# Optimization experiments

Hardware: AMD Instinct MI355X
Metric: run time of the kernel (lower is better)

The kernel has to match this reference:

```python
import jax, jax.numpy as jnp
import numpy as np

NUM_SAMPLES = 32
PATCH = 3
GROUP = 8
NUM_RUNS = 1
BOUNDARY_SHARE = 0.7


def setup_inputs() -> dict:
    key = jax.random.key(0)
    k1, k2 = jax.random.split(key)
    fmap = jax.random.normal(k1, (2, 64, 64, 64, 64), dtype=jnp.float32)
    mask = jax.random.randint(k2, (2, 64, 64, 64), 0, 2).astype(jnp.int32)
    return {"fmap": fmap, "mask": mask}


def _sample_k(key, probs, fallback, k, num_runs):
    # probs, fallback: (N, S). Returns (N, num_runs, k) indices sampled with replacement.
    n = probs.shape[0]
    if k == 0:
        return jnp.zeros((n, num_runs, 0), dtype=jnp.int32)
    probs = jnp.clip(jnp.nan_to_num(probs), 0.0, None)
    fb = jnp.clip(jnp.nan_to_num(fallback), 0.0, None)
    fb = jnp.where(fb.sum(axis=1, keepdims=True) == 0, 1.0, fb)  # fallback uniform if fb empty
    probs = jnp.where(probs.sum(axis=1, keepdims=True) == 0, fb, probs)
    logits = jnp.log(probs)  # -inf on zero prob entries; categorical handles unnormalized logits
    idx = jax.random.categorical(key, logits, shape=(num_runs * k, n)).T  # (N, num_runs*k)
    return idx.reshape(n, num_runs, k)


def _unravel_center(idx, H, W, r, Hp, Wp):
    # idx: flat index into unpadded (D,H,W) volume -> flat index of center in padded volume
    z = idx // (H * W)
    rem = idx % (H * W)
    y = rem // W
    x = rem % W
    return (z + r) * (Hp * Wp) + (y + r) * Wp + (x + r)


def reference(fmap, mask):
    B, C, D, H, W = fmap.shape
    g = GROUP
    G = C // g
    p = PATCH
    r = p // 2
    p3 = p ** 3
    ns = NUM_SAMPLES
    R = NUM_RUNS
    boundary_k = int(ns * BOUNDARY_SHARE)
    rest_k = ns - boundary_k

    maskf = mask.astype(jnp.float32)
    # replicate-pad feature map
    fmap_pad = jnp.pad(fmap, ((0, 0), (0, 0), (r, r), (r, r), (r, r)), mode='edge')
    Dp, Hp, Wp = D + 2 * r, H + 2 * r, W + 2 * r
    S_p = Dp * Hp * Wp

    # valid centers (interior)
    valid = jnp.zeros((B, D, H, W), dtype=bool).at[:, r:D - r, r:H - r, r:W - r].set(True)

    # boundary detection via 3x3x3 ones conv over the mask
    kernel = jnp.ones((1, 1, p, p, p), jnp.float32)
    counts = jax.lax.conv_general_dilated(
        maskf[:, None], kernel, (1, 1, 1), [(r, r)] * 3,
        dimension_numbers=('NCDHW', 'OIDHW', 'NCDHW'))[:, 0]

    pos_b = ((mask == 1) & (counts < p3)).reshape(B, -1).astype(jnp.float32)
    neg_b = ((mask == 0) & (counts > 0)).reshape(B, -1).astype(jnp.float32)
    pos = (mask == 1).reshape(B, -1).astype(jnp.float32)
    neg = (mask == 0).reshape(B, -1).astype(jnp.float32)
    validf = valid.reshape(B, -1).astype(jnp.float32)

    rep = lambda m: jnp.repeat(m, G, axis=0)  # (B,S) -> (B*G,S)

    keys = jax.random.split(jax.random.key(42), 4)
    pos_idx = jnp.concatenate([
        _sample_k(keys[0], rep(pos_b), rep(pos), boundary_k, R),
        _sample_k(keys[1], rep(pos), rep(validf), rest_k, R)], axis=2)
    neg_idx = jnp.concatenate([
        _sample_k(keys[2], rep(neg_b), rep(neg), boundary_k, R),
        _sample_k(keys[3], rep(neg), rep(validf), rest_k, R)], axis=2)
    pos_idx = pos_idx.reshape(B, G, R, ns)
    neg_idx = neg_idx.reshape(B, G, R, ns)

    # 3x3x3 neighborhood flat offsets in the padded volume
    d = jnp.arange(-r, r + 1)
    offs = (d[:, None, None] * (Hp * Wp) + d[None, :, None] * Wp + d[None, None, :]).reshape(-1)

    def gather_patches(idx):
        center = _unravel_center(idx, H, W, r, Hp, Wp)  # (B,G,R,ns)
        idxs = center[..., None] + offs  # (B,G,R,ns,p3)
        idxs_flat = idxs.reshape(B, G, 1, R * ns * p3)
        src = fmap_pad.reshape(B, G, g, S_p)
        patches = jnp.take_along_axis(src, idxs_flat, axis=3)  # (B,G,g,R*ns*p3)
        patches = patches.reshape(B, G, g, R, ns, p3).transpose(0, 1, 3, 4, 2, 5)
        return patches.reshape(B, G, R, ns * g * p3)

    pos_out = gather_patches(pos_idx)
    neg_out = gather_patches(neg_idx)
    return jnp.concatenate([pos_out, neg_out], axis=3)  # (B,G,R, 2*ns*g*p3)
```

## Files before the change

### kernel.cpp

```cpp
#include <hip/hip_runtime.h>
#include <stdint.h>


#define S_VOL   262144
#define VALID_N 238328
#define OUT_N   221184
#define CTR(b, set) (((b) * 4 + (set)) * 16)

struct Keys { uint32_t k[4][2]; };

#define TF_ROUND(r) { x0 += x1; x1 = (x1 << (r)) | (x1 >> (32 - (r))); x1 ^= x0; }

__host__ __device__ static inline void tf2x32(uint32_t k0, uint32_t k1,
                                              uint32_t& x0, uint32_t& x1) {
  uint32_t ks2 = k0 ^ k1 ^ 0x1BD11BDAu;
  x0 += k0; x1 += k1;
  TF_ROUND(13) TF_ROUND(15) TF_ROUND(26) TF_ROUND(6)
  x0 += k1;  x1 += ks2 + 1u;
  TF_ROUND(17) TF_ROUND(29) TF_ROUND(16) TF_ROUND(24)
  x0 += ks2; x1 += k0 + 2u;
  TF_ROUND(13) TF_ROUND(15) TF_ROUND(26) TF_ROUND(6)
  x0 += k0;  x1 += k1 + 3u;
  TF_ROUND(17) TF_ROUND(29) TF_ROUND(16) TF_ROUND(24)
  x0 += k1;  x1 += ks2 + 4u;
  TF_ROUND(13) TF_ROUND(15) TF_ROUND(26) TF_ROUND(6)
  x0 += ks2; x1 += k0 + 5u;
}

#define ROTL(x, r) __builtin_amdgcn_alignbit((x), (x), 32u - (r))
#define R4(a,b,c,d) { x0+=x1; x1=ROTL(x1,a); x1^=x0; \
                      x0+=x1; x1=ROTL(x1,b); x1^=x0; \
                      x0+=x1; x1=ROTL(x1,c); x1^=x0; \
                      x0+=x1; x1=ROTL(x1,d); x1^=x0; }

struct TFC { uint32_t x0i, sk1, a1,b1,a2,b2,a3,b3,a4,b4,a5,b5; };

__device__ static inline uint32_t tf_hash(uint32_t s, const TFC& c) {
  uint32_t x0 = c.x0i, x1 = s + c.sk1;
  R4(13,15,26,6)   x0 += c.a1; x1 += c.b1;
  R4(17,29,16,24)  x0 += c.a2; x1 += c.b2;
  R4(13,15,26,6)   x0 += c.a3; x1 += c.b3;
  R4(17,29,16,24)  x0 += c.a4; x1 += c.b4;
  R4(13,15,26,6)   x0 += c.a5; x1 += c.b5;
  return x0 ^ x1;
}

__device__ static inline unsigned long long shfl_down_u64(unsigned long long v, int off) {
  uint32_t lo = (uint32_t)v, hi = (uint32_t)(v >> 32);
  lo = __shfl_down(lo, off);
  hi = __shfl_down(hi, off);
  return ((unsigned long long)hi << 32) | lo;
}

__global__ __launch_bounds__(256) void k_compact(const int* __restrict__ mask,
                                                 int* __restrict__ ctr,
                                                 uint32_t* __restrict__ lists) {
  int t = blockIdx.x * 256 + threadIdx.x;
  int b = blockIdx.x >> 10;
  int s = t & (S_VOL - 1);
  int z = s >> 12, y = (s >> 6) & 63, x = s & 63;
  int m = mask[t];
  int cnt = 0;
  #pragma unroll
  for (int dz = -1; dz <= 1; ++dz) {
    int zz = z + dz; if (zz < 0 || zz > 63) continue;
    #pragma unroll
    for (int dy = -1; dy <= 1; ++dy) {
      int yy = y + dy; if (yy < 0 || yy > 63) continue;
      #pragma unroll
      for (int dx = -1; dx <= 1; ++dx) {
        int xx = x + dx; if (xx < 0 || xx > 63) continue;
        cnt += mask[(b << 18) + (zz << 12) + (yy << 6) + xx];
      }
    }
  }
  bool pred[4];
  pred[1] = (m == 1);
  pred[3] = (m == 0);
  pred[0] = pred[1] && (cnt < 27);
  pred[2] = pred[3] && (cnt > 0);

  __shared__ int wcnt[4][4];
  __shared__ int wbase[4][4];
  int wave = threadIdx.x >> 6;
  int lane = threadIdx.x & 63;
  unsigned long long below = (lane == 63) ? ~0ull : ((1ull << (lane + 1)) - 1ull);
  below >>= 1;

  int pre[4];
  #pragma unroll
  for (int set = 0; set < 4; ++set) {
    unsigned long long bv = __ballot(pred[set]);
    if (lane == 0) wcnt[set][wave] = (int)__popcll(bv);
    pre[set] = (int)__popcll(bv & below);
  }
  __syncthreads();
  if (threadIdx.x < 4) {
    int set = threadIdx.x;
    int c0 = wcnt[set][0], c1 = wcnt[set][1], c2 = wcnt[set][2], c3 = wcnt[set][3];
    int tot = c0 + c1 + c2 + c3;
    int base = 0;
    if (tot) base = atomicAdd(&ctr[CTR(b, set)], tot);
    wbase[set][0] = base;
    wbase[set][1] = base + c0;
    wbase[set][2] = base + c0 + c1;
    wbase[set][3] = base + c0 + c1 + c2;
  }
  __syncthreads();

  uint32_t* regA = lists + (size_t)b * (2 * S_VOL);
  uint32_t* regB = regA + S_VOL;
  #pragma unroll
  for (int set = 0; set < 4; ++set) {
    if (pred[set]) {
      int idx = wbase[set][wave] + pre[set];
      uint32_t* reg = (set & 1) ? regB : regA;
      reg[(set < 2) ? idx : (S_VOL - 1 - idx)] = (uint32_t)s;
    }
  }
}

__global__ void k_pad(const int* __restrict__ ctr, uint32_t* __restrict__ lists) {
  int i = threadIdx.x;
  if (i >= 8) return;
  int b = i >> 2, set = i & 3;
  uint32_t* regA = lists + (size_t)b * (2 * S_VOL);
  uint32_t* reg = (set & 1) ? regA + S_VOL : regA;
  int cnt = ctr[CTR(b, set)];
  if (cnt == 0 || cnt == S_VOL) return;
  if (set < 2) {
    uint32_t v = reg[0];
    for (int q = cnt; q < ((cnt + 3) & ~3); ++q) reg[q] = v;
  } else {
    int st = S_VOL - cnt;
    uint32_t v = reg[st];
    for (int q = (st & ~3); q < st; ++q) reg[q] = v;
  }
}

__global__ __launch_bounds__(256) void k_sample_list(const int* __restrict__ ctr,
                                                     const uint32_t* __restrict__ lists,
                                                     unsigned long long* __restrict__ slots,
                                                     Keys keys) {
  int wg = blockIdx.x;
  int chunk = wg & 1;
  int d = wg >> 1;
  int c, rem;
  if      (d < 352) { c = 0; rem = d; }
  else if (d < 512) { c = 1; rem = d - 352; }
  else if (d < 864) { c = 2; rem = d - 512; }
  else              { c = 3; rem = d - 864; }
  int n = rem & 15, j = rem >> 4;
  int b = n >> 3;

  int mode = 0, set = 0;
  if (c == 0)      { if (ctr[CTR(b,0)]) set = 0; else if (ctr[CTR(b,1)]) set = 1; else mode = 3; }
  else if (c == 1) { if (ctr[CTR(b,1)]) set = 1; else mode = 2; }
  else if (c == 2) { if (ctr[CTR(b,2)]) set = 2; else if (ctr[CTR(b,3)]) set = 3; else mode = 3; }
  else             { if (ctr[CTR(b,3)]) set = 3; else mode = 2; }

  uint32_t k0 = keys.k[c][0], k1 = keys.k[c][1];
  uint32_t ks2 = k0 ^ k1 ^ 0x1BD11BDAu;
  uint32_t ibase = (uint32_t)(j * 16 + n) * (uint32_t)S_VOL;
  TFC tc;
  tc.x0i = k0; tc.sk1 = ibase + k1;
  tc.a1 = k1;  tc.b1 = ks2 + 1u;
  tc.a2 = ks2; tc.b2 = k0 + 2u;
  tc.a3 = k0;  tc.b3 = k1 + 3u;
  tc.a4 = k1;  tc.b4 = ks2 + 4u;
  tc.a5 = ks2; tc.b5 = k0 + 5u;

  int tid = threadIdx.x;
  unsigned long long best = 0ull;

  if (mode == 0) {
    const uint32_t* regA = lists + (size_t)b * (2 * S_VOL);
    const uint32_t* reg = (set & 1) ? regA + S_VOL : regA;
    int cnt = ctr[CTR(b, set)];
    const uint32_t* base;
    int len4;
    if (set < 2) { base = reg; len4 = (cnt + 3) >> 2; }
    else { int st = (S_VOL - cnt) & ~3; base = reg + st; len4 = (S_VOL - st) >> 2; }
    const uint4* p4 = (const uint4*)base;
    for (uint32_t gi = (uint32_t)chunk; gi * 256u < (uint32_t)len4; gi += 2u) {
      uint32_t qi = gi * 256u + (uint32_t)tid;
      if (qi < (uint32_t)len4) {
        uint4 sv = p4[qi];
        #pragma unroll
        for (int u = 0; u < 4; ++u) {
          uint32_t s = (u == 0) ? sv.x : (u == 1) ? sv.y : (u == 2) ? sv.z : sv.w;
          uint32_t bits = tf_hash(s, tc);
          uint32_t vp = (bits >> 9) + 1u;
          unsigned long long key =
              ((unsigned long long)vp << 18) | (unsigned long long)((S_VOL - 1u) - s);
          best = best > key ? best : key;
        }
      }
    }
  } else if (mode == 2) {
    for (uint32_t i = (uint32_t)(chunk * 256 + tid); i < VALID_N; i += 512u) {
      uint32_t z = i / 3844u;
      uint32_t r2 = i - z * 3844u;
      uint32_t y = r2 / 62u;
      uint32_t x = r2 - y * 62u;
      uint32_t s = ((z + 1u) << 12) | ((y + 1u) << 6) | (x + 1u);
      uint32_t bits = tf_hash(s, tc);
      uint32_t vp = (bits >> 9) + 1u;
      unsigned long long key =
          ((unsigned long long)vp << 18) | (unsigned long long)((S_VOL - 1u) - s);
      best = best > key ? best : key;
    }
  } else {
    for (uint32_t s = (uint32_t)(chunk * 256 + tid); s < S_VOL; s += 512u) {
      uint32_t bits = tf_hash(s, tc);
      uint32_t vp = (bits >> 9) + 1u;
      unsigned long long key =
          ((unsigned long long)vp << 18) | (unsigned long long)((S_VOL - 1u) - s);
      best = best > key ? best : key;
    }
  }

  #pragma unroll
  for (int off = 32; off; off >>= 1) {
    unsigned long long o = shfl_down_u64(best, off);
    best = best > o ? best : o;
  }
  if ((tid & 63) == 0) atomicMax(&slots[d], best);
}

__global__ __launch_bounds__(256) void k_gather(const float* __restrict__ fmap,
                                                const unsigned long long* __restrict__ slots,
                                                float* __restrict__ out) {
  int tid = blockIdx.x * 256 + threadIdx.x;
  if (tid >= OUT_N) return;
  int o  = tid % 27;
  int q  = tid / 27;
  int cg = q & 7;   q >>= 3;
  int m  = q & 31;  q >>= 5;
  int t  = q & 1;   q >>= 1;
  int gi = q & 7;
  int b  = q >> 3;
  int n  = b * 8 + gi;
  int slot;
  if (t == 0) slot = (m < 22) ? (m * 16 + n) : (352 + (m - 22) * 16 + n);
  else        slot = (m < 22) ? (512 + m * 16 + n) : (864 + (m - 22) * 16 + n);
  int s = (S_VOL - 1) - (int)(slots[slot] & 0x3FFFFull);
  int z = s >> 12, y = (s >> 6) & 63, x = s & 63;
  int dz = o / 9 - 1, dy = (o / 3) % 3 - 1, dx = o % 3 - 1;
  int zc = min(max(z + dz, 0), 63);
  int yc = min(max(y + dy, 0), 63);
  int xc = min(max(x + dx, 0), 63);
  int ch = gi * 8 + cg;
  out[tid] = fmap[((b * 64 + ch) << 18) + (zc << 12) + (yc << 6) + xc];
}

extern "C" void kernel_launch(void* const* d_in, const int* in_sizes, int n_in,
                              void* d_out, int out_size, void* d_ws, size_t ws_size,
                              hipStream_t stream) {
  const float* fmap = (const float*)d_in[0];
  const int*   mask = (const int*)d_in[1];
  float* out = (float*)d_out;

  int* ctr = (int*)d_ws;
  unsigned long long* slots = (unsigned long long*)((char*)d_ws + 1024);
  uint32_t* lists = (uint32_t*)((char*)d_ws + 16384);

  Keys K;
  for (int c = 0; c < 4; ++c) {
    uint32_t x0 = 0u, x1 = (uint32_t)c;
    tf2x32(0u, 42u, x0, x1);
    K.k[c][0] = x0; K.k[c][1] = x1;
  }

  hipMemsetAsync(d_ws, 0, 16384, stream);
  hipLaunchKernelGGL(k_compact, dim3(2048), dim3(256), 0, stream, mask, ctr, lists);
  hipLaunchKernelGGL(k_pad, dim3(1), dim3(64), 0, stream, ctr, lists);
  hipLaunchKernelGGL(k_sample_list, dim3(2048), dim3(256), 0, stream, ctr, lists, slots, K);
  hipLaunchKernelGGL(k_gather, dim3((OUT_N + 255) / 256), dim3(256), 0, stream, fmap, slots, out);
}
```

Baseline: 305.4 us.

## Interleave two threefry hashes in inline asm and use 32-bit argmax tracking

The sampling kernel's hot loop now hashes two candidates at once with hand-written inline assembly, so two independent add/rotate/xor chains interleave and hide ALU latency. The 64-bit packed key max is replaced by a 32-bit value max plus a minimum-index tie-break. The list loads are software-prefetched one iteration ahead. The per-wave reduction shuffles two 32-bit values and builds the 64-bit key only once, before the atomic. The inline asm hard-codes rotate amounts written as alignbit shift counts, so exact threefry equivalence depends on those constants being right.

```diff
diff --git a/kernel.cpp b/kernel.cpp
--- a/kernel.cpp
+++ b/kernel.cpp
@@ -6,6 +6,7 @@
 #define VALID_N 238328
 #define OUT_N   221184
 #define CTR(b, set) (((b) * 4 + (set)) * 16)
+#define SINF 0xFFFFFFFFu
 
 struct Keys { uint32_t k[4][2]; };
 
@@ -27,29 +28,48 @@
   x0 += ks2; x1 += k0 + 5u;
 }
 
-#define ROTL(x, r) __builtin_amdgcn_alignbit((x), (x), 32u - (r))
-#define R4(a,b,c,d) { x0+=x1; x1=ROTL(x1,a); x1^=x0; \
-                      x0+=x1; x1=ROTL(x1,b); x1^=x0; \
-                      x0+=x1; x1=ROTL(x1,c); x1^=x0; \
-                      x0+=x1; x1=ROTL(x1,d); x1^=x0; }
-
 struct TFC { uint32_t x0i, sk1, a1,b1,a2,b2,a3,b3,a4,b4,a5,b5; };
 
-__device__ static inline uint32_t tf_hash(uint32_t s, const TFC& c) {
+__device__ static inline uint32_t tf_hash_c(uint32_t s, const TFC& c) {
   uint32_t x0 = c.x0i, x1 = s + c.sk1;
-  R4(13,15,26,6)   x0 += c.a1; x1 += c.b1;
-  R4(17,29,16,24)  x0 += c.a2; x1 += c.b2;
-  R4(13,15,26,6)   x0 += c.a3; x1 += c.b3;
-  R4(17,29,16,24)  x0 += c.a4; x1 += c.b4;
-  R4(13,15,26,6)   x0 += c.a5; x1 += c.b5;
+  #define RR(r) { x0 += x1; x1 = (x1 << (r)) | (x1 >> (32 - (r))); x1 ^= x0; }
+  RR(13) RR(15) RR(26) RR(6)   x0 += c.a1; x1 += c.b1;
+  RR(17) RR(29) RR(16) RR(24)  x0 += c.a2; x1 += c.b2;
+  RR(13) RR(15) RR(26) RR(6)   x0 += c.a3; x1 += c.b3;
+  RR(17) RR(29) RR(16) RR(24)  x0 += c.a4; x1 += c.b4;
+  RR(13) RR(15) RR(26) RR(6)   x0 += c.a5; x1 += c.b5;
+  #undef RR
   return x0 ^ x1;
 }
 
-__device__ static inline unsigned long long shfl_down_u64(unsigned long long v, int off) {
-  uint32_t lo = (uint32_t)v, hi = (uint32_t)(v >> 32);
-  lo = __shfl_down(lo, off);
-  hi = __shfl_down(hi, off);
-  return ((unsigned long long)hi << 32) | lo;
+#define RND2(S2) asm("v_add_u32 %0, %0, %1\n\t"                    \
+                     "v_add_u32 %2, %2, %3\n\t"                    \
+                     "v_alignbit_b32 %1, %1, %1, " #S2 "\n\t"      \
+                     "v_alignbit_b32 %3, %3, %3, " #S2 "\n\t"      \
+                     "v_xor_b32 %1, %1, %0\n\t"                    \
+                     "v_xor_b32 %3, %3, %2"                        \
+                     : "+v"(x0a), "+v"(x1a), "+v"(x0b), "+v"(x1b))
+#define GRP_A RND2(19); RND2(17); RND2(6); RND2(26)
+#define GRP_B RND2(15); RND2(3); RND2(16); RND2(8)
+
+#define HASH2(sa, sb, ba, bb) {                                         \
+  uint32_t x0a = tc.x0i, x1a = (sa) + tc.sk1;                           \
+  uint32_t x0b = tc.x0i, x1b = (sb) + tc.sk1;                           \
+  GRP_A; x0a += tc.a1; x1a += tc.b1; x0b += tc.a1; x1b += tc.b1;        \
+  GRP_B; x0a += tc.a2; x1a += tc.b2; x0b += tc.a2; x1b += tc.b2;        \
+  GRP_A; x0a += tc.a3; x1a += tc.b3; x0b += tc.a3; x1b += tc.b3;        \
+  GRP_B; x0a += tc.a4; x1a += tc.b4; x0b += tc.a4; x1b += tc.b4;        \
+  GRP_A; x0a += tc.a5; x1a += tc.b5; x0b += tc.a5; x1b += tc.b5;        \
+  ba = x0a ^ x1a; bb = x0b ^ x1b;                                       \
+}
+
+#define EPI(bits, s) {                                                  \
+  uint32_t v = (bits) >> 9;                                             \
+  bool gt = v > vmax;                                                   \
+  bool eq = v == vmax;                                                  \
+  uint32_t sm = smin < (s) ? smin : (s);                                \
+  vmax = gt ? v : vmax;                                                 \
+  smin = gt ? (s) : (eq ? sm : smin);                                   \
 }
 
 __global__ __launch_bounds__(256) void k_compact(const int* __restrict__ mask,
@@ -171,7 +191,7 @@
   tc.a5 = ks2; tc.b5 = k0 + 5u;
 
   int tid = threadIdx.x;
-  unsigned long long best = 0ull;
+  uint32_t vmax = 0u, smin = SINF;
 
   if (mode == 0) {
     const uint32_t* regA = lists + (size_t)b * (2 * S_VOL);
@@ -182,20 +202,28 @@
     if (set < 2) { base = reg; len4 = (cnt + 3) >> 2; }
     else { int st = (S_VOL - cnt) & ~3; base = reg + st; len4 = (S_VOL - st) >> 2; }
     const uint4* p4 = (const uint4*)base;
-    for (uint32_t gi = (uint32_t)chunk; gi * 256u < (uint32_t)len4; gi += 2u) {
-      uint32_t qi = gi * 256u + (uint32_t)tid;
-      if (qi < (uint32_t)len4) {
-        uint4 sv = p4[qi];
-        #pragma unroll
-        for (int u = 0; u < 4; ++u) {
-          uint32_t s = (u == 0) ? sv.x : (u == 1) ? sv.y : (u == 2) ? sv.z : sv.w;
-          uint32_t bits = tf_hash(s, tc);
-          uint32_t vp = (bits >> 9) + 1u;
-          unsigned long long key =
-              ((unsigned long long)vp << 18) | (unsigned long long)((S_VOL - 1u) - s);
-          best = best > key ? best : key;
-        }
-      }
+
+    int qi0 = chunk * 256 + tid;
+    int nt = (qi0 < len4) ? (((len4 - 1 - qi0) >> 9) + 1) : 0;
+    const uint4* p = p4 + qi0;
+    uint4 cv = {0, 0, 0, 0};
+    if (nt > 0) cv = *p;
+    for (int it = 0; it < nt - 1; ++it) {
+      p += 512;
+      uint4 nv = *p;
+      uint32_t ba, bb;
+      HASH2(cv.x, cv.y, ba, bb);
+      EPI(ba, cv.x); EPI(bb, cv.y);
+      HASH2(cv.z, cv.w, ba, bb);
+      EPI(ba, cv.z); EPI(bb, cv.w);
+      cv = nv;
+    }
+    if (nt > 0) {
+      uint32_t ba, bb;
+      HASH2(cv.x, cv.y, ba, bb);
+      EPI(ba, cv.x); EPI(bb, cv.y);
+      HASH2(cv.z, cv.w, ba, bb);
+      EPI(ba, cv.z); EPI(bb, cv.w);
     }
   } else if (mode == 2) {
     for (uint32_t i = (uint32_t)(chunk * 256 + tid); i < VALID_N; i += 512u) {
@@ -204,28 +232,30 @@
       uint32_t y = r2 / 62u;
       uint32_t x = r2 - y * 62u;
       uint32_t s = ((z + 1u) << 12) | ((y + 1u) << 6) | (x + 1u);
-      uint32_t bits = tf_hash(s, tc);
-      uint32_t vp = (bits >> 9) + 1u;
-      unsigned long long key =
-          ((unsigned long long)vp << 18) | (unsigned long long)((S_VOL - 1u) - s);
-      best = best > key ? best : key;
+      uint32_t bits = tf_hash_c(s, tc);
+      EPI(bits, s);
     }
   } else {
     for (uint32_t s = (uint32_t)(chunk * 256 + tid); s < S_VOL; s += 512u) {
-      uint32_t bits = tf_hash(s, tc);
-      uint32_t vp = (bits >> 9) + 1u;
-      unsigned long long key =
-          ((unsigned long long)vp << 18) | (unsigned long long)((S_VOL - 1u) - s);
-      best = best > key ? best : key;
+      uint32_t bits = tf_hash_c(s, tc);
+      EPI(bits, s);
     }
   }
 
   #pragma unroll
   for (int off = 32; off; off >>= 1) {
-    unsigned long long o = shfl_down_u64(best, off);
-    best = best > o ? best : o;
-  }
-  if ((tid & 63) == 0) atomicMax(&slots[d], best);
+    uint32_t ov = __shfl_down(vmax, off);
+    uint32_t os = __shfl_down(smin, off);
+    bool take = (ov > vmax) || (ov == vmax && os < smin);
+    vmax = take ? ov : vmax;
+    smin = take ? os : smin;
+  }
+  if ((tid & 63) == 0 && smin != SINF) {
+    unsigned long long key =
+        ((unsigned long long)(vmax + 1u) << 18) |
+        (unsigned long long)((S_VOL - 1u) - smin);
+    atomicMax(&slots[d], key);
+  }
 }
 
 __global__ __launch_bounds__(256) void k_gather(const float* __restrict__ fmap,
```

After: 309.3 us. Within noise of the previous version (+1.2%).
